# Kernel optimization log

Hardware: AMD Instinct MI355X
Metric: run time of the kernel (lower is better)

## Reference

```python
import jax, jax.numpy as jnp
import numpy as np

D_MODEL = 1024
NUM_HEADS = 16
HEAD_DIM = D_MODEL // NUM_HEADS
THETA = 10000.0
BATCH, SEQ = 2, 2048


def rope(x, token_positions):
    # x: [b, h, s, d]; token_positions: [s]
    d = x.shape[-1]
    freqs = 1.0 / THETA ** (jnp.arange(0, d, 2, dtype=jnp.float32)[: d // 2] / d)
    ang = token_positions.astype(jnp.float32)[:, None] * freqs[None, :]  # [s, d/2]
    cos, sin = jnp.cos(ang), jnp.sin(ang)
    xr = x.reshape(*x.shape[:-1], d // 2, 2)
    x_even, x_odd = xr[..., 0], xr[..., 1]
    out_even = x_even * cos - x_odd * sin
    out_odd = x_even * sin + x_odd * cos
    return jnp.stack([out_even, out_odd], axis=-1).reshape(x.shape)


def setup_inputs() -> dict:
    key = jax.random.key(0)
    ks = jax.random.split(key, 5)
    std = np.sqrt(2.0 / (D_MODEL + D_MODEL))
    mk = lambda k: (jax.random.truncated_normal(k, -3.0, 3.0, (D_MODEL, D_MODEL), jnp.float32) * std)
    return {
        "x": jax.random.normal(ks[0], (BATCH, SEQ, D_MODEL), jnp.float32),
        "Wq": mk(ks[1]),
        "Wk": mk(ks[2]),
        "Wv": mk(ks[3]),
        "Wo": mk(ks[4]),
        "casual_mask": jnp.tril(jnp.ones((SEQ, SEQ), dtype=bool)),
        "token_positions": jnp.arange(SEQ, dtype=jnp.int32),
    }


def reference(x, Wq, Wk, Wv, Wo, casual_mask, token_positions):
    b, s, _ = x.shape
    split = lambda t: t.reshape(b, s, NUM_HEADS, HEAD_DIM).transpose(0, 2, 1, 3)
    q = split(x @ Wq.T)  # [b, h, s, d]
    k = split(x @ Wk.T)
    v = split(x @ Wv.T)
    q = rope(q, token_positions)
    k = rope(k, token_positions)
    scores = jnp.einsum("bhqd,bhkd->bhqk", q, k) / np.sqrt(HEAD_DIM)
    scores = jnp.where(casual_mask, scores, -jnp.inf)
    probs = jax.nn.softmax(scores, axis=-1)
    out = jnp.einsum("bhqk,bhkd->bhqd", probs, v)
    out = out.transpose(0, 2, 1, 3).reshape(b, s, D_MODEL)
    return out @ Wo.T
```

## Files before the change

kernel.cpp:

```cpp
#include <hip/hip_runtime.h>
#include <hip/hip_bf16.h>

#define SEQ_LEN 2048
#define NBATCH 2
#define DM 1024
#define NH 16
#define HD 64
#define NR (NBATCH * SEQ_LEN)
#define NQKV (3 * DM)
#define LDQK 2048

typedef __attribute__((ext_vector_type(8))) short bf16x8;
typedef __attribute__((ext_vector_type(4))) float f32x4;
typedef __attribute__((ext_vector_type(16))) float f32x16;

__device__ __forceinline__ short f2b(float f) {
    __hip_bfloat16 h = __float2bfloat16(f);
    return *reinterpret_cast<short*>(&h);
}

__device__ __forceinline__ void gload_lds16(const void* g, void* l) {
    __builtin_amdgcn_global_load_lds(
        (const __attribute__((address_space(1))) unsigned int*)g,
        (__attribute__((address_space(3))) unsigned int*)l, 16, 0, 0);
}

__global__ __launch_bounds__(256) void cvt_all(
    const float* __restrict__ x,  const float* __restrict__ wq,
    const float* __restrict__ wk, const float* __restrict__ wv,
    const float* __restrict__ wo,
    __hip_bfloat16* __restrict__ xb, __hip_bfloat16* __restrict__ wqkvb,
    __hip_bfloat16* __restrict__ wob) {
    int id = blockIdx.x;
    const float* src; __hip_bfloat16* dst;
    if (id < 4096) { src = x + (size_t)id * 1024; dst = xb + (size_t)id * 1024; }
    else {
        int k = id - 4096, seg = k >> 10;
        size_t off = (size_t)(k & 1023) * 1024;
        if      (seg == 0) { src = wq + off; dst = wqkvb + off; }
        else if (seg == 1) { src = wk + off; dst = wqkvb + (1u << 20) + off; }
        else if (seg == 2) { src = wv + off; dst = wqkvb + (2u << 20) + off; }
        else               { src = wo + off; dst = wob + off; }
    }
    int i = threadIdx.x * 4;
    float4 v = *(const float4*)(src + i);
    dst[i + 0] = __float2bfloat16(v.x);
    dst[i + 1] = __float2bfloat16(v.y);
    dst[i + 2] = __float2bfloat16(v.z);
    dst[i + 3] = __float2bfloat16(v.w);
}

__device__ __forceinline__ void store_c(float* p, float v) { *p = v; }
__device__ __forceinline__ void store_c(__hip_bfloat16* p, float v) {
    *p = __float2bfloat16(v);
}

template <typename CT, bool FUSED>
__global__ __launch_bounds__(256) void gemm128(
    const __hip_bfloat16* __restrict__ A,
    const __hip_bfloat16* __restrict__ B,
    CT* __restrict__ C, int K, int ldc,
    __hip_bfloat16* __restrict__ Vtg, const int* __restrict__ pos) {
    __shared__ __hip_bfloat16 As[128 * 64];
    __shared__ __hip_bfloat16 Bs[128 * 64];
    const int t    = threadIdx.x;
    const int wave = t >> 6;
    const int lane = t & 63;
    const int quad = lane >> 4;
    const int l16  = lane & 15;
    const int wy = wave >> 1, wx = wave & 1;
    const int m0 = blockIdx.x * 128, n0 = blockIdx.y * 128;

    const int sr  = t >> 3;
    const int scx = (t & 7) ^ (sr & 7);

    const __hip_bfloat16* Ag = A + (size_t)(m0 + sr) * K + scx * 8;
    const __hip_bfloat16* Bg = B + (size_t)(n0 + sr) * K + scx * 8;

    f32x4 acc[4][4];
#pragma unroll
    for (int i = 0; i < 4; i++)
#pragma unroll
        for (int j = 0; j < 4; j++) acc[i][j] = (f32x4){0.f, 0.f, 0.f, 0.f};

    for (int k0 = 0; k0 < K; k0 += 64) {
        __syncthreads();
#pragma unroll
        for (int i = 0; i < 4; i++) {
            gload_lds16(Ag + (size_t)(i * 32) * K + k0, (char*)As + (t + i * 256) * 16);
            gload_lds16(Bg + (size_t)(i * 32) * K + k0, (char*)Bs + (t + i * 256) * 16);
        }
        __syncthreads();
#pragma unroll
        for (int kk = 0; kk < 2; kk++) {
            bf16x8 af[4], bfr[4];
#pragma unroll
            for (int rb = 0; rb < 4; rb++) {
                int row = wy * 64 + rb * 16 + l16;
                af[rb] = *(const bf16x8*)((const char*)As + row * 128 +
                                          (((kk * 4 + quad) ^ (row & 7)) << 4));
            }
#pragma unroll
            for (int cb = 0; cb < 4; cb++) {
                int row = wx * 64 + cb * 16 + l16;
                bfr[cb] = *(const bf16x8*)((const char*)Bs + row * 128 +
                                           (((kk * 4 + quad) ^ (row & 7)) << 4));
            }
#pragma unroll
            for (int rb = 0; rb < 4; rb++)
#pragma unroll
                for (int cb = 0; cb < 4; cb++)
                    acc[rb][cb] = __builtin_amdgcn_mfma_f32_16x16x32_bf16(
                        af[rb], bfr[cb], acc[rb][cb], 0, 0, 0);
        }
    }

    if (!FUSED || blockIdx.y < 16) {
        if constexpr (FUSED) {
            const float sc = (blockIdx.y < 8) ? 0.125f : 1.0f;
            float fr[4];
#pragma unroll
            for (int cb = 0; cb < 4; cb++) {
                int i = ((cb * 16 + l16) & 63) >> 1;
                fr[cb] = __expf(-(float)(2 * i) * (9.210340371976184f / 64.0f));
            }
            const float par = (l16 & 1) ? 1.f : -1.f;
#pragma unroll
            for (int rb = 0; rb < 4; rb++)
#pragma unroll
                for (int r = 0; r < 4; r++) {
                    int row = m0 + wy * 64 + rb * 16 + quad * 4 + r;
                    float p = (float)pos[row & (SEQ_LEN - 1)];
#pragma unroll
                    for (int cb = 0; cb < 4; cb++) {
                        float sn, cs;
                        __sincosf(p * fr[cb], &sn, &cs);
                        float v  = acc[rb][cb][r];
                        float pt = __shfl_xor(v, 1);
                        acc[rb][cb][r] = (v * cs + par * pt * sn) * sc;
                    }
                }
        }
#pragma unroll
        for (int rb = 0; rb < 4; rb++)
#pragma unroll
            for (int r = 0; r < 4; r++) {
                size_t ro = (size_t)(m0 + wy * 64 + rb * 16 + quad * 4 + r) * ldc;
#pragma unroll
                for (int cb = 0; cb < 4; cb++)
                    store_c(&C[ro + n0 + wx * 64 + cb * 16 + l16], acc[rb][cb][r]);
            }
    } else {
#pragma unroll
        for (int rb = 0; rb < 4; rb++) {
            int row0 = m0 + wy * 64 + rb * 16 + quad * 4;
            int bb = row0 >> 11, ss = row0 & (SEQ_LEN - 1);
            int ssw = (ss & ~12) | ((ss & 4) << 1) | ((ss & 8) >> 1);
#pragma unroll
            for (int cb = 0; cb < 4; cb++) {
                int vcol = n0 + wx * 64 + cb * 16 + l16 - 2048;
                int hh = vcol >> 6, dd = vcol & 63;
                ushort4 u;
                u.x = (unsigned short)f2b(acc[rb][cb][0]);
                u.y = (unsigned short)f2b(acc[rb][cb][1]);
                u.z = (unsigned short)f2b(acc[rb][cb][2]);
                u.w = (unsigned short)f2b(acc[rb][cb][3]);
                *(ushort4*)(Vtg + ((size_t)(bb * NH + hh) * HD + dd) * SEQ_LEN + ssw) = u;
            }
        }
    }
}

__global__ __launch_bounds__(256, 2) void attn_kernel(
    const __hip_bfloat16* __restrict__ QK,
    const __hip_bfloat16* __restrict__ Vtg,
    __hip_bfloat16* __restrict__ O) {
    __shared__ __hip_bfloat16 Ks[2][64 * 64];
    __shared__ __hip_bfloat16 Vs[2][64 * 64];

    const int t    = threadIdx.x;
    const int wave = t >> 6;
    const int lane = t & 63;
    const int l5   = lane & 31;
    const int hi   = lane >> 5;
    const int id   = blockIdx.x;
    const int qtc  = id >> 5;
    const int hb   = id & 31;
    const int h    = hb & 15;
    const int b    = hb >> 4;
    const int qt   = (qtc < 8) ? (15 - qtc) : (qtc - 8);

    const int row0 = qt * 128 + wave * 32;
    const int ktd  = (row0 + 31) >> 6;
    const int KTM  = 2 * qt + 1;

    const int sr  = t >> 3;
    const int scx = (t & 7) ^ (sr & 7);

    const __hip_bfloat16* kbase = QK + (size_t)(b * SEQ_LEN) * LDQK + DM + h * HD;
    const __hip_bfloat16* vbase = Vtg + (size_t)((b * NH + h) * HD) * SEQ_LEN;

    bf16x8 qf[4];
    {
        const __hip_bfloat16* qp =
            QK + (size_t)(b * SEQ_LEN + row0 + l5) * LDQK + h * HD + hi * 8;
#pragma unroll
        for (int dc = 0; dc < 4; dc++) qf[dc] = *(const bf16x8*)(qp + dc * 16);
    }

    f32x16 o0, o1;
#pragma unroll
    for (int i = 0; i < 16; i++) { o0[i] = 0.f; o1[i] = 0.f; }
    float l_acc = 0.f;

#define STAGE(BUF, KT)                                                          \
    {                                                                           \
        gload_lds16(kbase + (size_t)((KT) * 64 + sr) * LDQK + scx * 8,          \
                    (char*)&Ks[BUF][0] + t * 16);                               \
        gload_lds16(kbase + (size_t)((KT) * 64 + sr + 32) * LDQK + scx * 8,     \
                    (char*)&Ks[BUF][0] + (t + 256) * 16);                       \
        gload_lds16(vbase + (size_t)sr * SEQ_LEN + (KT) * 64 + scx * 8,         \
                    (char*)&Vs[BUF][0] + t * 16);                               \
        gload_lds16(vbase + (size_t)(sr + 32) * SEQ_LEN + (KT) * 64 + scx * 8,  \
                    (char*)&Vs[BUF][0] + (t + 256) * 16);                       \
    }

#define LFRAG(BASE, ROW, CH)                                                    \
    (*(const bf16x8*)((const char*)(BASE) + (ROW) * 128 + ((((CH) ^ ((ROW) & 7))) << 4)))

#define MKPA(S, PA0, PA1)                                                       \
    {                                                                           \
        float p_[16];                                                           \
        _Pragma("unroll") for (int r = 0; r < 16; r++) {                        \
            p_[r] = __expf((S)[r]);                                             \
            l_acc += p_[r];                                                     \
        }                                                                       \
        _Pragma("unroll") for (int j = 0; j < 8; j++) {                         \
            PA0[j] = f2b(p_[j]);                                                \
            PA1[j] = f2b(p_[8 + j]);                                            \
        }                                                                       \
    }

#define TRIP(BUF, KT)                                                           \
    {                                                                           \
        f32x16 s0, s1;                                                          \
        _Pragma("unroll") for (int i = 0; i < 16; i++) { s0[i] = 0.f; s1[i] = 0.f; } \
        __builtin_amdgcn_s_setprio(1);                                          \
        _Pragma("unroll") for (int dc = 0; dc < 4; dc++) {                      \
            bf16x8 k0f = LFRAG(Ks[BUF], l5, dc * 2 + hi);                       \
            bf16x8 k1f = LFRAG(Ks[BUF], 32 + l5, dc * 2 + hi);                  \
            s0 = __builtin_amdgcn_mfma_f32_32x32x16_bf16(k0f, qf[dc], s0, 0, 0, 0); \
            s1 = __builtin_amdgcn_mfma_f32_32x32x16_bf16(k1f, qf[dc], s1, 0, 0, 0); \
        }                                                                       \
        __builtin_amdgcn_s_setprio(0);                                          \
        if ((KT) == ktd) {                \
            int qrow = row0 + l5;                                               \
            _Pragma("unroll") for (int r = 0; r < 16; r++) {                    \
                int key = (KT) * 64 + (r & 3) + 8 * (r >> 2) + 4 * hi;          \
                if (key > qrow) s0[r] = -1e30f;                                 \
                if (key + 32 > qrow) s1[r] = -1e30f;                            \
            }                                                                   \
        }                                                                       \
        bf16x8 pa0, pa1, pa2, pa3;                                              \
        MKPA(s0, pa0, pa1);                                                     \
        MKPA(s1, pa2, pa3);                                                     \
        __builtin_amdgcn_s_setprio(1);                                          \
        _Pragma("unroll") for (int kc = 0; kc < 4; kc++) {                      \
            bf16x8 v0f = LFRAG(Vs[BUF], l5, kc * 2 + hi);                       \
            bf16x8 v1f = LFRAG(Vs[BUF], 32 + l5, kc * 2 + hi);                  \
            bf16x8 paf = (kc == 0) ? pa0 : (kc == 1) ? pa1 : (kc == 2) ? pa2 : pa3; \
            o0 = __builtin_amdgcn_mfma_f32_32x32x16_bf16(paf, v0f, o0, 0, 0, 0); \
            o1 = __builtin_amdgcn_mfma_f32_32x32x16_bf16(paf, v1f, o1, 0, 0, 0); \
        }                                                                       \
        __builtin_amdgcn_s_setprio(0);                                          \
    }

    STAGE(0, 0);
    for (int kt = 0; kt <= KTM; ++kt) {
        const int buf = kt & 1;
        __syncthreads();
        if (kt < KTM) STAGE(buf ^ 1, kt + 1);
        if (kt <= ktd) TRIP(buf, kt);
    }

    l_acc += __shfl_xor(l_acc, 32);
    float inv = 1.0f / l_acc;
#pragma unroll
    for (int r = 0; r < 16; r++) {
        int crow  = (r & 3) + 8 * (r >> 2) + 4 * hi;
        float invr = __shfl(inv, crow);
        size_t ro = (size_t)(b * SEQ_LEN + row0 + crow) * DM + h * HD;
        O[ro + l5]      = __float2bfloat16(o0[r] * invr);
        O[ro + 32 + l5] = __float2bfloat16(o1[r] * invr);
    }
#undef STAGE
#undef LFRAG
#undef MKPA
#undef TRIP
}

extern "C" void kernel_launch(void* const* d_in, const int* in_sizes, int n_in,
                              void* d_out, int out_size, void* d_ws, size_t ws_size,
                              hipStream_t stream) {
    const float* x  = (const float*)d_in[0];
    const float* Wq = (const float*)d_in[1];
    const float* Wk = (const float*)d_in[2];
    const float* Wv = (const float*)d_in[3];
    const float* Wo = (const float*)d_in[4];
    const int* pos = (const int*)d_in[6];
    float* out = (float*)d_out;

    char* w = (char*)d_ws;
    const size_t MiB = 1024 * 1024;
    __hip_bfloat16* xb    = (__hip_bfloat16*)(w + 0 * MiB);
    __hip_bfloat16* Ab    = (__hip_bfloat16*)(w + 0 * MiB);
    __hip_bfloat16* Wqkvb = (__hip_bfloat16*)(w + 8 * MiB);
    __hip_bfloat16* Wob   = (__hip_bfloat16*)(w + 14 * MiB);
    __hip_bfloat16* QKb   = (__hip_bfloat16*)(w + 16 * MiB);
    __hip_bfloat16* Vtg   = (__hip_bfloat16*)(w + 32 * MiB);

    cvt_all<<<8192, 256, 0, stream>>>(x, Wq, Wk, Wv, Wo, xb, Wqkvb, Wob);

    gemm128<__hip_bfloat16, true><<<dim3(NR / 128, NQKV / 128), 256, 0, stream>>>(
        xb, Wqkvb, QKb, DM, LDQK, Vtg, pos);

    attn_kernel<<<512, 256, 0, stream>>>(QKb, Vtg, Ab);

    gemm128<float, false><<<dim3(NR / 128, DM / 128), 256, 0, stream>>>(
        Ab, Wob, out, DM, DM, nullptr, nullptr);
}
```

Measured before the change: 200.9 us.

## Double-buffer GEMM LDS tiles with BK=32 and remap blocks across XCDs

The GEMM main loop now uses two 128x32 LDS buffers per operand and issues the next tile's global-to-LDS loads before computing the current one, so memory latency overlaps MFMA work. This removes one barrier per iteration. The grid becomes 1D and block indices are permuted in groups of 8 so that neighbouring tiles land on the same XCD, aiming at better L2 reuse. Costs: a smaller K tile means more iterations and barriers, and the swizzle is now 4-way.

```diff
diff --git a/kernel.cpp b/kernel.cpp
--- a/kernel.cpp
+++ b/kernel.cpp
@@ -60,64 +60,77 @@
     const __hip_bfloat16* __restrict__ A,
     const __hip_bfloat16* __restrict__ B,
     CT* __restrict__ C, int K, int ldc,
-    __hip_bfloat16* __restrict__ Vtg, const int* __restrict__ pos) {
-    __shared__ __hip_bfloat16 As[128 * 64];
-    __shared__ __hip_bfloat16 Bs[128 * 64];
+    __hip_bfloat16* __restrict__ Vtg, const int* __restrict__ pos, int nbx) {
+    __shared__ __hip_bfloat16 As[2][128 * 32];
+    __shared__ __hip_bfloat16 Bs[2][128 * 32];
     const int t    = threadIdx.x;
     const int wave = t >> 6;
     const int lane = t & 63;
     const int quad = lane >> 4;
     const int l16  = lane & 15;
     const int wy = wave >> 1, wx = wave & 1;
-    const int m0 = blockIdx.x * 128, n0 = blockIdx.y * 128;
-
-    const int sr  = t >> 3;
-    const int scx = (t & 7) ^ (sr & 7);
+
+    const int nwg = gridDim.x;
+    const int wg  = (blockIdx.x & 7) * (nwg >> 3) + (blockIdx.x >> 3);
+    const int bx  = wg % nbx;
+    const int by  = wg / nbx;
+    const int m0 = bx * 128, n0 = by * 128;
+
+    const int sr  = t >> 2;
+    const int scx = (t & 3) ^ (sr & 3);
 
     const __hip_bfloat16* Ag = A + (size_t)(m0 + sr) * K + scx * 8;
     const __hip_bfloat16* Bg = B + (size_t)(n0 + sr) * K + scx * 8;
 
+#define GSTAGE(BUF, K0)                                                         \
+    {                                                                           \
+        gload_lds16(Ag + (K0), (char*)As[BUF] + t * 16);                        \
+        gload_lds16(Ag + (size_t)64 * K + (K0), (char*)As[BUF] + (t + 256) * 16); \
+        gload_lds16(Bg + (K0), (char*)Bs[BUF] + t * 16);                        \
+        gload_lds16(Bg + (size_t)64 * K + (K0), (char*)Bs[BUF] + (t + 256) * 16); \
+    }
+
     f32x4 acc[4][4];
 #pragma unroll
     for (int i = 0; i < 4; i++)
 #pragma unroll
         for (int j = 0; j < 4; j++) acc[i][j] = (f32x4){0.f, 0.f, 0.f, 0.f};
 
-    for (int k0 = 0; k0 < K; k0 += 64) {
+    const int NT = K >> 5;
+    GSTAGE(0, 0);
+    __syncthreads();
+    int cur = 0;
+    for (int t32 = 0; t32 < NT; ++t32) {
+        if (t32 + 1 < NT) GSTAGE(cur ^ 1, (t32 + 1) * 32);
+
+        bf16x8 af[4], bfr[4];
+#pragma unroll
+        for (int rb = 0; rb < 4; rb++) {
+            int row = wy * 64 + rb * 16 + l16;
+            af[rb] = *(const bf16x8*)((const char*)As[cur] + row * 64 +
+                                      ((quad ^ (row & 3)) << 4));
+        }
+#pragma unroll
+        for (int cb = 0; cb < 4; cb++) {
+            int row = wx * 64 + cb * 16 + l16;
+            bfr[cb] = *(const bf16x8*)((const char*)Bs[cur] + row * 64 +
+                                       ((quad ^ (row & 3)) << 4));
+        }
+#pragma unroll
+        for (int rb = 0; rb < 4; rb++)
+#pragma unroll
+            for (int cb = 0; cb < 4; cb++)
+                acc[rb][cb] = __builtin_amdgcn_mfma_f32_16x16x32_bf16(
+                    af[rb], bfr[cb], acc[rb][cb], 0, 0, 0);
+
         __syncthreads();
-#pragma unroll
-        for (int i = 0; i < 4; i++) {
-            gload_lds16(Ag + (size_t)(i * 32) * K + k0, (char*)As + (t + i * 256) * 16);
-            gload_lds16(Bg + (size_t)(i * 32) * K + k0, (char*)Bs + (t + i * 256) * 16);
-        }
-        __syncthreads();
-#pragma unroll
-        for (int kk = 0; kk < 2; kk++) {
-            bf16x8 af[4], bfr[4];
-#pragma unroll
-            for (int rb = 0; rb < 4; rb++) {
-                int row = wy * 64 + rb * 16 + l16;
-                af[rb] = *(const bf16x8*)((const char*)As + row * 128 +
-                                          (((kk * 4 + quad) ^ (row & 7)) << 4));
-            }
-#pragma unroll
-            for (int cb = 0; cb < 4; cb++) {
-                int row = wx * 64 + cb * 16 + l16;
-                bfr[cb] = *(const bf16x8*)((const char*)Bs + row * 128 +
-                                           (((kk * 4 + quad) ^ (row & 7)) << 4));
-            }
-#pragma unroll
-            for (int rb = 0; rb < 4; rb++)
-#pragma unroll
-                for (int cb = 0; cb < 4; cb++)
-                    acc[rb][cb] = __builtin_amdgcn_mfma_f32_16x16x32_bf16(
-                        af[rb], bfr[cb], acc[rb][cb], 0, 0, 0);
-        }
-    }
-
-    if (!FUSED || blockIdx.y < 16) {
+        cur ^= 1;
+    }
+#undef GSTAGE
+
+    if (!FUSED || by < 16) {
         if constexpr (FUSED) {
-            const float sc = (blockIdx.y < 8) ? 0.125f : 1.0f;
+            const float sc = (by < 8) ? 0.125f : 1.0f;
             float fr[4];
 #pragma unroll
             for (int cb = 0; cb < 4; cb++) {
@@ -321,11 +334,11 @@
 
     cvt_all<<<8192, 256, 0, stream>>>(x, Wq, Wk, Wv, Wo, xb, Wqkvb, Wob);
 
-    gemm128<__hip_bfloat16, true><<<dim3(NR / 128, NQKV / 128), 256, 0, stream>>>(
-        xb, Wqkvb, QKb, DM, LDQK, Vtg, pos);
+    gemm128<__hip_bfloat16, true><<<(NR / 128) * (NQKV / 128), 256, 0, stream>>>(
+        xb, Wqkvb, QKb, DM, LDQK, Vtg, pos, NR / 128);
 
     attn_kernel<<<512, 256, 0, stream>>>(QKb, Vtg, Ab);
 
-    gemm128<float, false><<<dim3(NR / 128, DM / 128), 256, 0, stream>>>(
-        Ab, Wob, out, DM, DM, nullptr, nullptr);
-}
+    gemm128<float, false><<<(NR / 128) * (DM / 128), 256, 0, stream>>>(
+        Ab, Wob, out, DM, DM, nullptr, nullptr, NR / 128);
+}
```

Measured after the change: 196.5 us. -2.2%, faster.
